# Performance work log

Hardware: AMD Instinct MI355X
Metric: run time of the kernel (lower is better)

Reference implementation:

```python
import jax, jax.numpy as jnp
import numpy as np

EPS = 1e-5


def _resize_bilinear_ac(x, h, w):
    # bilinear, align_corners=True; x: [B, C, H, W]
    H, W = x.shape[2], x.shape[3]
    ys = jnp.linspace(0.0, H - 1.0, h)
    xs = jnp.linspace(0.0, W - 1.0, w)
    y0 = jnp.floor(ys).astype(jnp.int32)
    x0 = jnp.floor(xs).astype(jnp.int32)
    y1 = jnp.clip(y0 + 1, 0, H - 1)
    x1 = jnp.clip(x0 + 1, 0, W - 1)
    wy = (ys - y0.astype(ys.dtype))[None, None, :, None]
    wx = (xs - x0.astype(xs.dtype))[None, None, None, :]
    rows0 = x[:, :, y0, :]  # [B,C,h,W]
    rows1 = x[:, :, y1, :]
    a = rows0[:, :, :, x0]
    b = rows0[:, :, :, x1]
    c = rows1[:, :, :, x0]
    d = rows1[:, :, :, x1]
    top = a * (1.0 - wx) + b * wx
    bot = c * (1.0 - wx) + d * wx
    return top * (1.0 - wy) + bot * wy


def _conv3x3(x, w):
    return jax.lax.conv_general_dilated(
        x, w, window_strides=(1, 1), padding=[(1, 1), (1, 1)],
        dimension_numbers=('NCHW', 'OIHW', 'NCHW'))


def _bn(x, g, b, m, v):
    scale = (g / jnp.sqrt(v + EPS))[None, :, None, None]
    shift = (b - m * g / jnp.sqrt(v + EPS))[None, :, None, None]
    return x * scale + shift


def setup_inputs() -> dict:
    key = jax.random.key(0)
    ks = jax.random.split(key, 12)
    B = 8
    xt = jax.random.normal(ks[0], (B, 512, 32, 32), jnp.float32)
    xm = jax.random.normal(ks[1], (B, 512, 64, 64), jnp.float32)
    xl = jax.random.normal(ks[2], (B, 256, 128, 128), jnp.float32)
    alpha = jnp.ones((1,), jnp.float32)
    w0 = jax.random.normal(ks[3], (512, 512, 3, 3), jnp.float32) * 0.02
    g0 = jnp.abs(jax.random.normal(ks[4], (512,), jnp.float32)) * 0.1 + 1.0
    b0 = jax.random.normal(ks[5], (512,), jnp.float32) * 0.1
    m0 = jax.random.normal(ks[6], (512,), jnp.float32) * 0.1
    v0 = jnp.abs(jax.random.normal(ks[7], (512,), jnp.float32)) * 0.1 + 1.0
    w1 = jax.random.normal(ks[8], (256, 512, 3, 3), jnp.float32) * 0.02
    g1 = jnp.abs(jax.random.normal(ks[9], (256,), jnp.float32)) * 0.1 + 1.0
    b1 = jax.random.normal(ks[10], (256,), jnp.float32) * 0.1
    m1 = jax.random.normal(ks[11], (256,), jnp.float32) * 0.1
    v1 = jnp.abs(jax.random.normal(jax.random.fold_in(key, 99), (256,), jnp.float32)) * 0.1 + 1.0
    return {"xt": xt, "xm": xm, "xl": xl, "alpha": alpha,
            "w0": w0, "g0": g0, "b0": b0, "m0": m0, "v0": v0,
            "w1": w1, "g1": g1, "b1": b1, "m1": m1, "v1": v1}


def reference(xt, xm, xl, alpha, w0, g0, b0, m0, v0, w1, g1, b1, m1, v1):
    # DecoderModule.forward: upsample xt to xm size (align_corners=True),
    # fuse with alpha-weighted skip, conv0(512->512,BN,ReLU), conv1(512->256,BN,ReLU).
    # xl is accepted but unused in this forward (as in the source).
    h, w = xm.shape[2], xm.shape[3]
    xup = _resize_bilinear_ac(xt, h, w)
    xfuse = xup + alpha[0] * xm
    x = jax.nn.relu(_bn(_conv3x3(xfuse, w0), g0, b0, m0, v0))
    xt_fea = jax.nn.relu(_bn(_conv3x3(x, w1), g1, b1, m1, v1))
    return xt_fea
```

## Files before the change

### kernel.cpp

```cpp
#include <hip/hip_runtime.h>
#include <stdint.h>

#define EPSV 1e-5f

#define CPLANE 278784

using floatx4 = __attribute__((ext_vector_type(4))) float;
using short8  = __attribute__((ext_vector_type(8))) short;

#define GLD(gp, lp) __builtin_amdgcn_global_load_lds( \
    (const __attribute__((address_space(1))) void*)(gp), \
    (__attribute__((address_space(3))) void*)(lp), 16, 0, 0)

__device__ __forceinline__ unsigned short f2bf(float f) {
  union { float f; unsigned int u; } x; x.f = f;
  unsigned int r = x.u + 0x7fffu + ((x.u >> 16) & 1u);
  return (unsigned short)(r >> 16);
}

__global__ __launch_bounds__(256) void border_zero_kernel(
    unsigned short* __restrict__ Xp0, unsigned short* __restrict__ Xp1) {
  int idx = blockIdx.x * 256 + threadIdx.x;
  int k = idx % 260;
  int rest = idx / 260;
  int cc = rest & 63;
  int b = rest >> 6;
  int py, px;
  if (k < 66)       { py = 0;  px = k; }
  else if (k < 132) { py = 65; px = k - 66; }
  else { int k2 = k - 132; py = 1 + (k2 >> 1); px = (k2 & 1) ? 65 : 0; }
  int off = cc * CPLANE + ((b * 66 + py) * 66 + px) * 8;
  short8 z = {};
  *(short8*)(Xp0 + off) = z;
  *(short8*)(Xp1 + off) = z;
}

__global__ __launch_bounds__(256) void fuse_upsample_kernel(
    const float* __restrict__ xt, const float* __restrict__ xm,
    const float* __restrict__ alpha, unsigned short* __restrict__ Xp) {
  __shared__ float sm[32 * 66];
  __shared__ float st[2 * 32 * 34];

  const int tid = threadIdx.x;
  const int ct = blockIdx.x & 15;
  const int y  = (blockIdx.x >> 4) & 63;
  const int b  = blockIdx.x >> 10;
  const int c0 = ct * 32;

  const float fy = y * (31.0f / 63.0f);
  const int y0 = (int)fy;
  const float wy = fy - (float)y0;
  const int y1 = min(y0 + 1, 31);

  {
    const int cb = (tid >> 6) * 8;
    const int xi = tid & 63;
#pragma unroll
    for (int j = 0; j < 8; ++j) {
      int c = cb + j;
      sm[c * 66 + xi] = xm[(((b << 9) + c0 + c) << 12) + (y << 6) + xi];
    }
  }
#pragma unroll
  for (int j = 0; j < 8; ++j) {
    int idx = j * 256 + tid;
    int xi = idx & 31, cc = (idx >> 5) & 31, h = idx >> 10;
    int yr = h ? y1 : y0;
    st[h * 1088 + cc * 34 + xi] =
        xt[(((b << 9) + c0 + cc) << 10) + (yr << 5) + xi];
  }
  __syncthreads();

  const float a = alpha[0];
  const int xo = tid & 63;
  const int cl = tid >> 6;
  const float fx = xo * (31.0f / 63.0f);
  const int x0 = (int)fx;
  const float wx = fx - (float)x0;
  const int x1 = min(x0 + 1, 31);
  short8 ov;
#pragma unroll
  for (int j = 0; j < 8; ++j) {
    int c = cl * 8 + j;
    float t0 = st[c * 34 + x0], t1 = st[c * 34 + x1];
    float u0 = st[1088 + c * 34 + x0], u1 = st[1088 + c * 34 + x1];
    float top = t0 * (1.0f - wx) + t1 * wx;
    float bot = u0 * (1.0f - wx) + u1 * wx;
    float up = top * (1.0f - wy) + bot * wy;
    float val = up + a * sm[c * 66 + xo];
    ov[j] = (short)f2bf(val);
  }
  *(short8*)(Xp + ((c0 >> 3) + cl) * CPLANE +
             ((b * 66 + y + 1) * 66 + xo + 1) * 8) = ov;
}

template <int COUT>
__global__ __launch_bounds__(256) void prep_w_kernel(
    const float* __restrict__ w, unsigned short* __restrict__ Wg) {
  __shared__ unsigned short l[4608];
  const int o = blockIdx.x, t = threadIdx.x;
  const float* src = w + o * 4608;
#pragma unroll
  for (int j = 0; j < 18; ++j) {
    int idx = j * 256 + t;
    l[(idx % 9) * 512 + idx / 9] = f2bf(src[idx]);
  }
  __syncthreads();
#pragma unroll
  for (int tap = 0; tap < 9; ++tap) {
    int cc = t >> 2;
    int off = ((tap * 64 + cc) * COUT + o) * 8 + ((2 * t) & 7);
    *(unsigned int*)(Wg + off) = *(const unsigned int*)(l + (tap << 9) + 2 * t);
  }
}

template <int COUT, int CTILE, bool FINAL>
__global__ __launch_bounds__(256, 2) void conv3x3_kernel(
    const unsigned short* __restrict__ Xp, const unsigned short* __restrict__ Wg,
    const float* __restrict__ gamma, const float* __restrict__ beta,
    const float* __restrict__ mean, const float* __restrict__ var,
    unsigned short* __restrict__ OutPad, float* __restrict__ OutF) {
  constexpr int NCT = COUT / CTILE;
  constexpr int NI  = CTILE / 32;
  constexpr int KCS = 2128;
  constexpr int ABUF = 8 * KCS;
  __shared__ __align__(64) unsigned short Abuf[2][ABUF];

  const int tid = threadIdx.x;
  const int ptile = (int)blockIdx.x / NCT;
  const int ctile = (int)blockIdx.x % NCT;
  const int p0 = ptile * 128;
  const int w = tid >> 6;
  const int lane = tid & 63;

  const int pb = p0 >> 12;
  const int yb = (p0 >> 6) & 63;
  const int arowg = ((pb * 66 + yb) * 66) * 8;

  const int fi = lane & 15;
  const int kc = lane >> 4;
  const int wm = w >> 1, wn = w & 1;
  const int aLane = kc * KCS + (wm + 1) * 528 + (fi + 1) * 8;

  floatx4 acc[4][NI] = {};
  short8 bcur[2][NI], bnxt[2][NI];

  auto stageA = [&](int cg, int bsel) {
#pragma unroll
    for (int kk = 0; kk < 2; ++kk) {
      const int kc2 = 2 * w + kk;
      const unsigned short* g = Xp + (cg * 8 + kc2) * CPLANE + arowg + lane * 8;
      unsigned short* d = &Abuf[bsel][0] + kc2 * KCS;
#pragma unroll
      for (int rr = 0; rr < 4; ++rr) {
        GLD(g + rr * 528,      d + rr * 528);
        GLD(g + rr * 528 + 16, d + rr * 528 + 16);
      }
    }
  };

  auto loadB = [&](int tap, int cg, short8 (&dst)[2][NI]) {
    const unsigned short* base =
        Wg + ((tap * 64 + cg * 8 + kc) * COUT +
              ctile * CTILE + wn * (CTILE / 2) + fi) * 8;
#pragma unroll
    for (int t = 0; t < 2; ++t)
#pragma unroll
      for (int ni = 0; ni < NI; ++ni)
        dst[t][ni] = *(const short8*)(base + (t * 4 * COUT + ni * 16) * 8);
  };

  auto compute = [&](int bsel, int dy, int dx) {
    const unsigned short* ab = &Abuf[bsel][0] + aLane + dy * 528 + dx * 8;
#pragma unroll
    for (int t = 0; t < 2; ++t) {
      short8 af[4];
#pragma unroll
      for (int mi = 0; mi < 4; ++mi)
        af[mi] = *(const short8*)(ab + t * (4 * KCS) + mi * 128);
#pragma unroll
      for (int mi = 0; mi < 4; ++mi)
#pragma unroll
        for (int ni = 0; ni < NI; ++ni)
          acc[mi][ni] = __builtin_amdgcn_mfma_f32_16x16x32_bf16(
              af[mi], bcur[t][ni], acc[mi][ni], 0, 0, 0);
    }
  };

  stageA(0, 0);
  loadB(0, 0, bcur);
  __syncthreads();

  int cur = 0;
  for (int cg = 0; cg < 8; ++cg) {
    if (cg < 7) stageA(cg + 1, cur ^ 1);
#pragma unroll
    for (int tap = 0; tap < 9; ++tap) {
      if (tap < 8)      loadB(tap + 1, cg, bnxt);
      else if (cg < 7)  loadB(0, cg + 1, bnxt);
      compute(cur, tap / 3 - 1, tap % 3 - 1);
#pragma unroll
      for (int t = 0; t < 2; ++t)
#pragma unroll
        for (int ni = 0; ni < NI; ++ni) bcur[t][ni] = bnxt[t][ni];
    }
    __syncthreads();
    cur ^= 1;
  }

#pragma unroll
  for (int ni = 0; ni < NI; ++ni) {
    const int co = ctile * CTILE + wn * (CTILE / 2) + ni * 16 + fi;
    const float sc = gamma[co] / sqrtf(var[co] + EPSV);
    const float sh2 = beta[co] - mean[co] * sc;
#pragma unroll
    for (int mi = 0; mi < 4; ++mi) {
      const int p = p0 + wm * 64 + mi * 16 + kc * 4;
      const int pbb = p >> 12;
      const int prem = p & 4095;
      if constexpr (FINAL) {
        floatx4 o;
#pragma unroll
        for (int r = 0; r < 4; ++r) o[r] = fmaxf(acc[mi][ni][r] * sc + sh2, 0.0f);
        *(floatx4*)(OutF + ((pbb * COUT + co) << 12) + prem) = o;
      } else {
        const int py = prem >> 6, px = prem & 63;
        unsigned short* dst = OutPad + (co >> 3) * CPLANE +
            ((pbb * 66 + py + 1) * 66 + px + 1) * 8 + (co & 7);
#pragma unroll
        for (int r = 0; r < 4; ++r)
          dst[r * 8] = f2bf(fmaxf(acc[mi][ni][r] * sc + sh2, 0.0f));
      }
    }
  }
}

extern "C" void kernel_launch(void* const* d_in, const int* in_sizes, int n_in,
                              void* d_out, int out_size, void* d_ws, size_t ws_size,
                              hipStream_t stream) {
  const float* xt    = (const float*)d_in[0];
  const float* xm    = (const float*)d_in[1];
  const float* alpha = (const float*)d_in[3];
  const float* w0    = (const float*)d_in[4];
  const float* g0    = (const float*)d_in[5];
  const float* b0    = (const float*)d_in[6];
  const float* m0    = (const float*)d_in[7];
  const float* v0    = (const float*)d_in[8];
  const float* w1    = (const float*)d_in[9];
  const float* g1    = (const float*)d_in[10];
  const float* b1    = (const float*)d_in[11];
  const float* m1    = (const float*)d_in[12];
  const float* v1    = (const float*)d_in[13];
  float* out = (float*)d_out;

  char* ws = (char*)d_ws;
  unsigned short* Xp0 = (unsigned short*)(ws);
  unsigned short* Xp1 = (unsigned short*)(ws + 35684352);
  unsigned short* Wg0 = (unsigned short*)(ws + 2 * 35684352);
  unsigned short* Wg1 = (unsigned short*)(ws + 2 * 35684352 + 4718592);

  border_zero_kernel<<<520, 256, 0, stream>>>(Xp0, Xp1);
  prep_w_kernel<512><<<512, 256, 0, stream>>>(w0, Wg0);
  prep_w_kernel<256><<<256, 256, 0, stream>>>(w1, Wg1);
  fuse_upsample_kernel<<<8192, 256, 0, stream>>>(xt, xm, alpha, Xp0);
  conv3x3_kernel<512, 128, false><<<1024, 256, 0, stream>>>(Xp0, Wg0, g0, b0, m0, v0, Xp1, nullptr);
  conv3x3_kernel<256, 64, true><<<1024, 256, 0, stream>>>(Xp1, Wg1, g1, b1, m1, v1, nullptr, out);
}
```

Baseline: 544.4 us.

## Ping-pong B registers without copies and widen second conv channel tile

The B-fragment double buffer now alternates between two register sets by tap parity, and the channel-group loop is unrolled by two so the roles stay consistent. This removes the per-tap register copy from bnxt to bcur. The second conv launch also moves from a 64-wide to a 128-wide output-channel tile with half the blocks, which reuses each staged A tile across more channels. The cost is higher register pressure from NI doubling and fewer blocks, which may lower occupancy.

```diff
diff --git a/kernel.cpp b/kernel.cpp
--- a/kernel.cpp
+++ b/kernel.cpp
@@ -143,7 +143,9 @@
   const int aLane = kc * KCS + (wm + 1) * 528 + (fi + 1) * 8;
 
   floatx4 acc[4][NI] = {};
-  short8 bcur[2][NI], bnxt[2][NI];
+  short8 B0[2][NI], B1[2][NI];
+
+  int cur = 0;
 
   auto stageA = [&](int cg, int bsel) {
 #pragma unroll
@@ -170,8 +172,12 @@
         dst[t][ni] = *(const short8*)(base + (t * 4 * COUT + ni * 16) * 8);
   };
 
-  auto compute = [&](int bsel, int dy, int dx) {
-    const unsigned short* ab = &Abuf[bsel][0] + aLane + dy * 528 + dx * 8;
+  auto tapStep = [&](int cg, int tap, short8 (&bc)[2][NI],
+                     short8 (&bn)[2][NI]) {
+    if (tap < 8)      loadB(tap + 1, cg, bn);
+    else if (cg < 7)  loadB(0, cg + 1, bn);
+    const int dy = tap / 3 - 1, dx = tap % 3 - 1;
+    const unsigned short* ab = &Abuf[cur][0] + aLane + dy * 528 + dx * 8;
 #pragma unroll
     for (int t = 0; t < 2; ++t) {
       short8 af[4];
@@ -183,26 +189,29 @@
 #pragma unroll
         for (int ni = 0; ni < NI; ++ni)
           acc[mi][ni] = __builtin_amdgcn_mfma_f32_16x16x32_bf16(
-              af[mi], bcur[t][ni], acc[mi][ni], 0, 0, 0);
+              af[mi], bc[t][ni], acc[mi][ni], 0, 0, 0);
     }
   };
 
   stageA(0, 0);
-  loadB(0, 0, bcur);
+  loadB(0, 0, B0);
   __syncthreads();
 
-  int cur = 0;
-  for (int cg = 0; cg < 8; ++cg) {
-    if (cg < 7) stageA(cg + 1, cur ^ 1);
+  for (int cgp = 0; cgp < 4; ++cgp) {
+    const int cg = 2 * cgp;
+    stageA(cg + 1, cur ^ 1);
 #pragma unroll
     for (int tap = 0; tap < 9; ++tap) {
-      if (tap < 8)      loadB(tap + 1, cg, bnxt);
-      else if (cg < 7)  loadB(0, cg + 1, bnxt);
-      compute(cur, tap / 3 - 1, tap % 3 - 1);
-#pragma unroll
-      for (int t = 0; t < 2; ++t)
-#pragma unroll
-        for (int ni = 0; ni < NI; ++ni) bcur[t][ni] = bnxt[t][ni];
+      if ((tap & 1) == 0) tapStep(cg, tap, B0, B1);
+      else                tapStep(cg, tap, B1, B0);
+    }
+    __syncthreads();
+    cur ^= 1;
+    if (cg + 2 < 8) stageA(cg + 2, cur ^ 1);
+#pragma unroll
+    for (int tap = 0; tap < 9; ++tap) {
+      if ((tap & 1) == 0) tapStep(cg + 1, tap, B1, B0);
+      else                tapStep(cg + 1, tap, B0, B1);
     }
     __syncthreads();
     cur ^= 1;
@@ -264,5 +273,5 @@
   prep_w_kernel<256><<<256, 256, 0, stream>>>(w1, Wg1);
   fuse_upsample_kernel<<<8192, 256, 0, stream>>>(xt, xm, alpha, Xp0);
   conv3x3_kernel<512, 128, false><<<1024, 256, 0, stream>>>(Xp0, Wg0, g0, b0, m0, v0, Xp1, nullptr);
-  conv3x3_kernel<256, 64, true><<<1024, 256, 0, stream>>>(Xp1, Wg1, g1, b1, m1, v1, nullptr, out);
-}
+  conv3x3_kernel<256, 128, true><<<512, 256, 0, stream>>>(Xp1, Wg1, g1, b1, m1, v1, nullptr, out);
+}
```

After: 504.9 us. -7.2%, faster.
